# Optimization experiments

Hardware: AMD Instinct MI355X
Metric: run time of the kernel (lower is better)

Reference implementation:

```python
import jax, jax.numpy as jnp
import numpy as np

# dims
B, N = 8, 64            # graphs, nodes per graph (equal-size ragged batch)
IN_DIM, EDGE_DIM = 16, 8
D, H = 128, 4
DH = D // H             # 32
L = 3                   # num_layers
FF = 4 * D              # 512
OUT = 1
SCALE = float(np.sqrt(DH))


def setup_inputs() -> dict:
    key = jax.random.key(0)
    ks = jax.random.split(key, 24)
    w = lambda k, s: jax.random.normal(k, s, jnp.float32) * 0.02
    return {
        'x': jax.random.normal(ks[0], (B, N, IN_DIM), jnp.float32),
        'edge_attr': jax.random.normal(ks[1], (B, N, N, EDGE_DIM), jnp.float32),
        'edge_mask': jax.random.bernoulli(ks[2], 0.2, (B, N, N)),
        # feature encoder (linear node + linear edge encoders, learned no-edge token)
        'node_W': w(ks[3], (IN_DIM, D)), 'node_b': jnp.zeros((D,), jnp.float32),
        'edge_W': w(ks[4], (EDGE_DIM, D)), 'edge_b': jnp.zeros((D,), jnp.float32),
        'no_edge': w(ks[5], (D,)),
        # per-layer edge-transformer params (stacked over L for lax.scan)
        'Wq': w(ks[6], (L, D, D)), 'Wk': w(ks[7], (L, D, D)),
        'Wv1': w(ks[8], (L, D, D)), 'Wv2': w(ks[9], (L, D, D)),
        'Wo': w(ks[10], (L, D, D)), 'bo': jnp.zeros((L, D), jnp.float32),
        'ln1_g': jnp.ones((L, D), jnp.float32), 'ln1_b': jnp.zeros((L, D), jnp.float32),
        'W1': w(ks[11], (L, D, FF)), 'b1': jnp.zeros((L, FF), jnp.float32),
        'W2': w(ks[12], (L, FF, D)), 'b2': jnp.zeros((L, D), jnp.float32),
        'ln2_g': jnp.ones((L, D), jnp.float32), 'ln2_b': jnp.zeros((L, D), jnp.float32),
        'Wout': w(ks[13], (D, OUT)), 'bout': jnp.zeros((OUT,), jnp.float32),
    }


def _ln(t, g, b):
    m = t.mean(-1, keepdims=True)
    v = t.var(-1, keepdims=True)
    return (t - m) * jax.lax.rsqrt(v + 1e-5) * g + b


def _forward(x, edge_attr, edge_mask, node_W, node_b, edge_W, edge_b, no_edge,
             Wq, Wk, Wv1, Wv2, Wo, bo, ln1_g, ln1_b, W1, b1, W2, b2,
             ln2_g, ln2_b, Wout, bout):
    # feature encoding: pair-token grid [B,N,N,D]
    node_emb = x @ node_W + node_b                       # [B,N,D]
    edge_emb = edge_attr @ edge_W + edge_b               # [B,N,N,D]
    tok = jnp.where(edge_mask[..., None], edge_emb, no_edge)
    eye = jnp.eye(N, dtype=bool)
    tok = jnp.where(eye[None, :, :, None], node_emb[:, :, None, :], tok)

    def heads(t, W):
        return (t @ W).reshape(B, N, N, H, DH)

    def layer(tok, p):
        wq, wk, wv1, wv2, wo, bo_, g1, b1_, w1, bf1, w2, bf2, g2, b2_ = p
        q = heads(tok, wq); k = heads(tok, wk)
        v1 = heads(tok, wv1); v2 = heads(tok, wv2)
        # triangular attention: token (i,j) attends over intermediate l
        s = jnp.einsum('bilhd,bljhd->bhilj', q, k) / SCALE   # [B,H,N,N,N]
        a = jax.nn.softmax(s, axis=3)                        # softmax over l
        o = jnp.einsum('bhilj,bilhd,bljhd->bijhd', a, v1, v2).reshape(B, N, N, D)
        tok = _ln(tok + o @ wo + bo_, g1, b1_)
        f = jax.nn.relu(tok @ w1 + bf1) @ w2 + bf2
        tok = _ln(tok + f, g2, b2_)
        return tok, None

    tok, _ = jax.lax.scan(
        layer, tok,
        (Wq, Wk, Wv1, Wv2, Wo, bo, ln1_g, ln1_b, W1, b1, W2, b2, ln2_g, ln2_b))

    diag = tok[:, jnp.arange(N), jnp.arange(N), :]           # node tokens [B,N,D]
    return diag @ Wout + bout                                 # [B,N,OUT]


def reference(x, edge_attr, edge_mask, node_W, node_b, edge_W, edge_b, no_edge,
              Wq, Wk, Wv1, Wv2, Wo, bo, ln1_g, ln1_b, W1, b1, W2, b2,
              ln2_g, ln2_b, Wout, bout):
    return _forward(x, edge_attr, edge_mask, node_W, node_b, edge_W, edge_b,
                    no_edge, Wq, Wk, Wv1, Wv2, Wo, bo, ln1_g, ln1_b,
                    W1, b1, W2, b2, ln2_g, ln2_b, Wout, bout)
```

## Files before the change

kernel.cpp:

```cpp
#include <hip/hip_runtime.h>

typedef unsigned short u16;
typedef __attribute__((ext_vector_type(8))) short bf16x8;
typedef __attribute__((ext_vector_type(4))) float f32x4;

#define INV_SCALE 0.17677669529663687f

static __device__ __forceinline__ float b2f(u16 u) {
    union { unsigned int i; float f; } v; v.i = ((unsigned int)u) << 16; return v.f;
}
static __device__ __forceinline__ u16 f2b(float f) {
    union { float f; unsigned int i; } v; v.f = f;
    unsigned int r = (v.i + 0x7FFFu + ((v.i >> 16) & 1u)) >> 16;
    return (u16)r;
}

#define NSEG 23
__device__ __constant__ int d_seg_off[NSEG + 1] = {
    0, 8192, 270336, 272384, 272512, 273536, 273664, 273792, 322944, 372096,
    421248, 470400, 519552, 519936, 520320, 520704, 717312, 718848, 915456,
    915840, 916224, 916608, 916736, 916744};
static const int h_seg_off[NSEG + 1] = {
    0, 8192, 270336, 272384, 272512, 273536, 273664, 273792, 322944, 372096,
    421248, 470400, 519552, 519936, 520320, 520704, 717312, 718848, 915456,
    915840, 916224, 916608, 916736, 916744};
#define ARENA_TOTAL 916744

struct ParamPtrs { const void* p[NSEG]; };

__global__ __launch_bounds__(256) void convert_params(ParamPtrs pp, u16* __restrict__ arena,
                                                      const void* __restrict__ mask,
                                                      int* __restrict__ mode) {
    if (blockIdx.x == 0) {
        __shared__ int f16, f32s, u8s;
        int tid = threadIdx.x;
        if (tid == 0) { f16 = 0; f32s = 0; u8s = 0; }
        __syncthreads();
        const u16* mu = (const u16*)mask;
        const unsigned int* mw = (const unsigned int*)mask;
        if (mu[2 * tid] == 0x3F80u) atomicOr(&f16, 1);
        if (mw[tid] == 0x3F800000u) atomicOr(&f32s, 1);
        if (mw[tid] > 1u) atomicOr(&u8s, 1);
        __syncthreads();
        if (tid == 0) mode[0] = f16 ? 0 : (f32s ? 3 : (u8s ? 1 : 2));
    }
    const unsigned int probe = ((const unsigned int*)pp.p[13])[0];
    const bool f32 = (probe == 0x3F800000u);
    for (int e = blockIdx.x * 256 + threadIdx.x; e < ARENA_TOTAL; e += gridDim.x * 256) {
        int k = 0;
        #pragma unroll
        for (int s2 = 1; s2 < NSEG; ++s2) if (e >= d_seg_off[s2]) k = s2;
        int local = e - d_seg_off[k];
        u16 v;
        if (k == 22 && local >= 1) v = 0;
        else v = f32 ? f2b(((const float*)pp.p[k])[local]) : ((const u16*)pp.p[k])[local];
        arena[e] = v;
    }
}

__global__ __launch_bounds__(256) void assemble_kernel(
    const u16* __restrict__ x, const u16* __restrict__ ea,
    const void* __restrict__ mask, const int* __restrict__ modeptr,
    const u16* __restrict__ nodeW, const u16* __restrict__ nodeB,
    const u16* __restrict__ edgeW, const u16* __restrict__ edgeB, const u16* __restrict__ noedge,
    float* __restrict__ tokf, u16* __restrict__ tokb)
{
    const int md = modeptr[0];
    int g = blockIdx.x * 256 + threadIdx.x;
    int t = g >> 5, dq = g & 31, d0 = dq * 4;
    int b = t >> 12, i = (t >> 6) & 63, j = t & 63;
    float v[4];
    if (i == j) {
        #pragma unroll
        for (int c = 0; c < 4; c++) v[c] = b2f(nodeB[d0 + c]);
        #pragma unroll
        for (int e = 0; e < 16; e++) {
            float xe = b2f(x[(b * 64 + i) * 16 + e]);
            #pragma unroll
            for (int c = 0; c < 4; c++) v[c] += xe * b2f(nodeW[e * 128 + d0 + c]);
        }
    } else {
        bool edge;
        if (md == 0)      edge = ((const u16*)mask)[t] != 0;
        else if (md == 3) edge = ((const float*)mask)[t] != 0.0f;
        else if (md == 1) edge = ((const unsigned char*)mask)[t] != 0;
        else              edge = ((const unsigned int*)mask)[t] != 0;
        if (edge) {
            #pragma unroll
            for (int c = 0; c < 4; c++) v[c] = b2f(edgeB[d0 + c]);
            #pragma unroll
            for (int e = 0; e < 8; e++) {
                float ae = b2f(ea[t * 8 + e]);
                #pragma unroll
                for (int c = 0; c < 4; c++) v[c] += ae * b2f(edgeW[e * 128 + d0 + c]);
            }
        } else {
            #pragma unroll
            for (int c = 0; c < 4; c++) v[c] = b2f(noedge[d0 + c]);
        }
    }
    *(float4*)(tokf + (size_t)t * 128 + d0) = make_float4(v[0], v[1], v[2], v[3]);
    u16 pk[4];
    #pragma unroll
    for (int c = 0; c < 4; c++) pk[c] = f2b(v[c]);
    *(uint2*)(tokb + (size_t)t * 128 + d0) = *(uint2*)pk;
}

__global__ __launch_bounds__(256) void gemm_kernel(
    const u16* __restrict__ A, int lda,
    const u16* __restrict__ B0, const u16* __restrict__ B1,
    const u16* __restrict__ B2, const u16* __restrict__ B3,
    int ldb, const u16* __restrict__ bias,
    int K, int mode,
    u16* __restrict__ outb, int ldc,
    float* __restrict__ tokf,
    u16* __restrict__ qb, u16* __restrict__ kb, u16* __restrict__ v2b,
    const u16* __restrict__ lng, const u16* __restrict__ lnb, u16* __restrict__ tokbO)
{
    __shared__ __align__(16) u16 smem[2 * 128 * 72];
    u16* As = smem;
    u16* Bs = smem + 128 * 72;
    int tid = threadIdx.x;
    int m0 = blockIdx.x * 128;
    int by = blockIdx.y;
    const u16* Bp; int c0;
    if (mode == 3) { Bp = (by == 0) ? B0 : (by == 1) ? B1 : (by == 2) ? B2 : B3; c0 = 0; }
    else { Bp = B0; c0 = by * 128; }

    int w = tid >> 6, lane = tid & 63;
    int q = lane >> 4, r16 = lane & 15;
    int rw = (w >> 1) * 64, cw = (w & 1) * 64;

    f32x4 acc[4][4];
    #pragma unroll
    for (int mi = 0; mi < 4; mi++)
        #pragma unroll
        for (int ni = 0; ni < 4; ni++) acc[mi][ni] = (f32x4){0.f, 0.f, 0.f, 0.f};

    int nkt = K >> 6;
    for (int kt = 0; kt < nkt; ++kt) {
        int k0 = kt * 64;
        __syncthreads();
        #pragma unroll
        for (int it = 0; it < 4; ++it) {
            int idx = tid + it * 256;
            int row = idx >> 3, ch = idx & 7;
            uint4 d = *(const uint4*)(A + (size_t)(m0 + row) * lda + k0 + ch * 8);
            *(uint4*)&As[row * 72 + ch * 8] = d;
        }
        #pragma unroll
        for (int it = 0; it < 4; ++it) {
            int idx = tid + it * 256;
            int kk = idx >> 4, nc = idx & 15;
            uint4 d = *(const uint4*)(Bp + (size_t)(k0 + kk) * ldb + c0 + nc * 8);
            const u16* ds = (const u16*)&d;
            int chunk = kk >> 3, kin = kk & 7;
            #pragma unroll
            for (int e = 0; e < 8; ++e) {
                int n = nc * 8 + e;
                int ch2 = chunk ^ ((n >> 3) & 7);
                Bs[n * 72 + ch2 * 8 + kin] = ds[e];
            }
        }
        __syncthreads();
        #pragma unroll
        for (int ks = 0; ks < 2; ++ks) {
            bf16x8 fa[4], fb[4];
            #pragma unroll
            for (int mi = 0; mi < 4; mi++)
                fa[mi] = *(const bf16x8*)&As[(rw + mi * 16 + r16) * 72 + ks * 32 + q * 8];
            #pragma unroll
            for (int ni = 0; ni < 4; ni++) {
                int n = cw + ni * 16 + r16;
                int ch2 = (ks * 4 + q) ^ ((n >> 3) & 7);
                fb[ni] = *(const bf16x8*)&Bs[n * 72 + ch2 * 8];
            }
            #pragma unroll
            for (int mi = 0; mi < 4; mi++)
                #pragma unroll
                for (int ni = 0; ni < 4; ni++)
                    acc[mi][ni] = __builtin_amdgcn_mfma_f32_16x16x32_bf16(fa[mi], fb[ni], acc[mi][ni], 0, 0, 0);
        }
    }

    int bl = m0 >> 12, it0 = (m0 >> 6) & 63;
    __syncthreads();
    if (mode == 4) {
        float* cf  = (float*)smem;
        float* rsm = cf + 128 * 64;
        float* rqm = rsm + 256;
        int half = cw >> 6;
        #pragma unroll
        for (int ni = 0; ni < 4; ni++) {
            int col = cw + ni * 16 + r16;
            float bb = b2f(bias[col]);
            #pragma unroll
            for (int mi = 0; mi < 4; mi++)
                #pragma unroll
                for (int rr = 0; rr < 4; rr++) {
                    int r = rw + mi * 16 + q * 4 + rr;
                    acc[mi][ni][rr] += bb + tokf[(size_t)(m0 + r) * 128 + col];
                }
        }
        #pragma unroll
        for (int mi = 0; mi < 4; mi++)
            #pragma unroll
            for (int rr = 0; rr < 4; rr++) {
                float s = 0.f, sq = 0.f;
                #pragma unroll
                for (int ni = 0; ni < 4; ni++) { float t = acc[mi][ni][rr]; s += t; sq += t * t; }
                #pragma unroll
                for (int off = 1; off < 16; off <<= 1) {
                    s  += __shfl_xor(s,  off, 16);
                    sq += __shfl_xor(sq, off, 16);
                }
                if (r16 == 0) {
                    int r = rw + mi * 16 + q * 4 + rr;
                    rsm[half * 128 + r] = s;
                    rqm[half * 128 + r] = sq;
                }
            }
        __syncthreads();
        float gl[4], bv[4];
        #pragma unroll
        for (int ni = 0; ni < 4; ni++) {
            int col = cw + ni * 16 + r16;
            gl[ni] = b2f(lng[col]);
            bv[ni] = b2f(lnb[col]);
        }
        #pragma unroll
        for (int mi = 0; mi < 4; mi++)
            #pragma unroll
            for (int rr = 0; rr < 4; rr++) {
                int r = rw + mi * 16 + q * 4 + rr;
                float tot = rsm[r] + rsm[128 + r];
                float tq  = rqm[r] + rqm[128 + r];
                float mean = tot * 0.0078125f;
                float var  = tq * 0.0078125f - mean * mean;
                float rstd = rsqrtf(var + 1e-5f);
                #pragma unroll
                for (int ni = 0; ni < 4; ni++)
                    acc[mi][ni][rr] = (acc[mi][ni][rr] - mean) * rstd * gl[ni] + bv[ni];
            }
        #pragma unroll
        for (int hp = 0; hp < 2; ++hp) {
            __syncthreads();
            if (half == hp) {
                #pragma unroll
                for (int mi = 0; mi < 4; mi++)
                    #pragma unroll
                    for (int ni = 0; ni < 4; ni++) {
                        int colh = (cw & 63) + ni * 16 + r16;
                        int ch4 = colh >> 2, cl = colh & 3;
                        #pragma unroll
                        for (int rr = 0; rr < 4; rr++) {
                            int r = rw + mi * 16 + q * 4 + rr;
                            cf[r * 64 + (((ch4 ^ (r & 15)) << 2) | cl)] = acc[mi][ni][rr];
                        }
                    }
            }
            __syncthreads();
            #pragma unroll
            for (int it = 0; it < 8; ++it) {
                int idx = tid + it * 256;
                int r = idx >> 4, c4 = idx & 15;
                f32x4 v = *(const f32x4*)&cf[r * 64 + ((c4 ^ (r & 15)) << 2)];
                int col = hp * 64 + c4 * 4;
                *(f32x4*)(tokf + (size_t)(m0 + r) * 128 + col) = v;
                u16 pk[4];
                #pragma unroll
                for (int e = 0; e < 4; e++) pk[e] = f2b(v[e]);
                *(uint2*)(tokbO + (size_t)(m0 + r) * 128 + col) = *(uint2*)pk;
            }
        }
    } else if (mode == 3 && by == 2) {
        float* cf = (float*)smem;
        #pragma unroll
        for (int hp = 0; hp < 2; ++hp) {
            if (hp) __syncthreads();
            if ((cw >> 6) == hp) {
                #pragma unroll
                for (int mi = 0; mi < 4; mi++) {
                    #pragma unroll
                    for (int ni = 0; ni < 4; ni++) {
                        int colh = (cw & 63) + ni * 16 + r16;
                        int ch4 = colh >> 2, cl = colh & 3;
                        #pragma unroll
                        for (int rr = 0; rr < 4; rr++) {
                            int r = rw + mi * 16 + q * 4 + rr;
                            cf[r * 64 + (((ch4 ^ (r & 15)) << 2) | cl)] = acc[mi][ni][rr];
                        }
                    }
                }
            }
            __syncthreads();
            #pragma unroll
            for (int it = 0; it < 8; ++it) {
                int idx = tid + it * 256;
                int hh = idx >> 10, itl = (idx >> 9) & 1, jt = (idx >> 3) & 63, d4 = idx & 7;
                int r = itl * 64 + jt;
                int colh = hh * 32 + d4 * 4;
                f32x4 v = *(const f32x4*)&cf[r * 64 + (((colh >> 2) ^ (r & 15)) << 2)];
                int h = hp * 2 + hh;
                *(f32x4*)&tokf[((((size_t)(bl * 4 + h)) * 64 + it0 + itl) * 64 + jt) * 32 + d4 * 4] = v;
            }
        }
    } else {
        u16* cs = smem;
        #pragma unroll
        for (int mi = 0; mi < 4; mi++) {
            #pragma unroll
            for (int ni = 0; ni < 4; ni++) {
                int col = cw + ni * 16 + r16;
                int ch = col >> 3, cl = col & 7;
                #pragma unroll
                for (int rr = 0; rr < 4; rr++) {
                    int r = rw + mi * 16 + q * 4 + rr;
                    float v = acc[mi][ni][rr];
                    if (mode == 1) { v += b2f(bias[c0 + col]); v = fmaxf(v, 0.f); }
                    cs[r * 128 + (((ch ^ (r & 15)) << 3) | cl)] = f2b(v);
                }
            }
        }
        __syncthreads();
        if (mode == 1) {
            #pragma unroll
            for (int it = 0; it < 8; ++it) {
                int idx = tid + it * 256;
                int r = idx >> 4, c8 = idx & 15;
                uint4 d = *(const uint4*)&cs[r * 128 + ((c8 ^ (r & 15)) << 3)];
                *(uint4*)&outb[(size_t)(m0 + r) * ldc + c0 + c8 * 8] = d;
            }
        } else if (by == 0) {
            #pragma unroll
            for (int it = 0; it < 8; ++it) {
                int idx = tid + it * 256;
                int h = idx >> 9, jt = (idx >> 3) & 63, itl = (idx >> 2) & 1, d8 = idx & 3;
                int r = itl * 64 + jt, c8 = h * 4 + d8;
                uint4 d = *(const uint4*)&cs[r * 128 + ((c8 ^ (r & 15)) << 3)];
                *(uint4*)&qb[((((size_t)(bl * 4 + h)) * 64 + jt) * 64 + it0 + itl) * 32 + d8 * 8] = d;
            }
        } else {
            u16* dp = (by == 1) ? kb : v2b;
            #pragma unroll
            for (int it = 0; it < 8; ++it) {
                int idx = tid + it * 256;
                int h = idx >> 9, itl = (idx >> 8) & 1, jt = (idx >> 2) & 63, d8 = idx & 3;
                int r = itl * 64 + jt, c8 = h * 4 + d8;
                uint4 d = *(const uint4*)&cs[r * 128 + ((c8 ^ (r & 15)) << 3)];
                *(uint4*)&dp[((((size_t)(bl * 4 + h)) * 64 + it0 + itl) * 64 + jt) * 32 + d8 * 8] = d;
            }
        }
    }
}

__global__ __launch_bounds__(64) void attn_s_kernel(
    const u16* __restrict__ qb, const u16* __restrict__ kb, u16* __restrict__ s)
{
    __shared__ __align__(16) u16 qs[64 * 40];
    __shared__ __align__(16) u16 ks_[64 * 40];
    int g = blockIdx.x;
    int l = g & 63, bh = g >> 6;
    const u16* Q = qb + ((size_t)bh * 64 + l) * 2048;
    const u16* Kp = kb + ((size_t)bh * 64 + l) * 2048;
    int lane = threadIdx.x;
    #pragma unroll
    for (int it = 0; it < 4; ++it) {
        int idx = lane + it * 64;
        int row = idx >> 2, c4 = idx & 3;
        *(uint4*)&qs[row * 40 + c4 * 8] = *(const uint4*)(Q + row * 32 + c4 * 8);
        *(uint4*)&ks_[row * 40 + c4 * 8] = *(const uint4*)(Kp + row * 32 + c4 * 8);
    }
    __syncthreads();
    int q = lane >> 4, r16 = lane & 15;
    f32x4 acc[4][4];
    #pragma unroll
    for (int mi = 0; mi < 4; mi++)
        #pragma unroll
        for (int ni = 0; ni < 4; ni++) acc[mi][ni] = (f32x4){0.f, 0.f, 0.f, 0.f};
    bf16x8 fa[4], fb[4];
    #pragma unroll
    for (int mi = 0; mi < 4; mi++) fa[mi] = *(const bf16x8*)&qs[(mi * 16 + r16) * 40 + q * 8];
    #pragma unroll
    for (int ni = 0; ni < 4; ni++) fb[ni] = *(const bf16x8*)&ks_[(ni * 16 + r16) * 40 + q * 8];
    #pragma unroll
    for (int mi = 0; mi < 4; mi++)
        #pragma unroll
        for (int ni = 0; ni < 4; ni++)
            acc[mi][ni] = __builtin_amdgcn_mfma_f32_16x16x32_bf16(fa[mi], fb[ni], acc[mi][ni], 0, 0, 0);
    u16* sb = s + (size_t)bh * 262144 + l * 64;
    #pragma unroll
    for (int mi = 0; mi < 4; mi++)
        #pragma unroll
        for (int ni = 0; ni < 4; ni++)
            #pragma unroll
            for (int rr = 0; rr < 4; rr++) {
                int i = mi * 16 + q * 4 + rr, j = ni * 16 + r16;
                sb[(size_t)i * 4096 + j] = f2b(acc[mi][ni][rr] * INV_SCALE);
            }
}

__global__ __launch_bounds__(512) void attn_o_kernel(
    const u16* __restrict__ a, const float* __restrict__ v1f, const u16* __restrict__ v2b,
    u16* __restrict__ ob)
{
    __shared__ __align__(16) float v2s[4 * 2304];
    __shared__ __align__(16) u16   as_[8 * 4 * 64];
    __shared__ __align__(16) float v1s[8 * 4 * 32];
    int bh = blockIdx.x;
    int i0 = blockIdx.y * 8;
    int bl = bh >> 2, h = bh & 3;
    int tid = threadIdx.x;
    int w = __builtin_amdgcn_readfirstlane(tid >> 6);
    int j = tid & 63;
    int ih = w & 1;
    int dh = (w >> 1) * 8;
    const u16*   v2base = v2b + (size_t)bh * 131072;
    const float* v1base = v1f + (size_t)bh * 131072 + (size_t)i0 * 2048;
    const u16*   abase  = a + (size_t)bh * 262144 + (size_t)i0 * 4096;

    uint4 pv2[2]; unsigned pa[2]; float pv1[2];
    int ia[2], la[2], ja[2], iv[2], lv[2], dv[2], lz[2], jz[2], cz[2];
    #pragma unroll
    for (int it = 0; it < 2; ++it) {
        int idx = tid + it * 512;
        lz[it] = idx >> 8; jz[it] = (idx >> 2) & 63; cz[it] = idx & 3;
        ia[it] = idx >> 7; la[it] = (idx >> 5) & 3; ja[it] = idx & 31;
        iv[it] = idx >> 7; lv[it] = (idx >> 5) & 3; dv[it] = idx & 31;
    }

#define LOAD_CHUNK(l0_)                                                             \
    _Pragma("unroll")                                                               \
    for (int it = 0; it < 2; ++it) {                                                \
        pv2[it] = *(const uint4*)(v2base + ((size_t)((l0_) + lz[it]) * 64 + jz[it]) * 32 + cz[it] * 8); \
        pa[it]  = *(const unsigned*)(abase + (size_t)ia[it] * 4096 + ((l0_) + la[it]) * 64 + ja[it] * 2); \
        pv1[it] = v1base[(size_t)iv[it] * 2048 + ((l0_) + lv[it]) * 32 + dv[it]];   \
    }

#define STORE_CHUNK()                                                               \
    _Pragma("unroll")                                                               \
    for (int it = 0; it < 2; ++it) {                                                \
        const u16* ds = (const u16*)&pv2[it];                                       \
        float* dst = &v2s[lz[it] * 2304 + jz[it] * 36 + cz[it] * 8];                \
        _Pragma("unroll")                                                           \
        for (int e = 0; e < 8; e++) dst[e] = b2f(ds[e]);                            \
        *(unsigned*)&as_[ia[it] * 256 + la[it] * 64 + ja[it] * 2] = pa[it];         \
        v1s[iv[it] * 128 + lv[it] * 32 + dv[it]] = pv1[it];                         \
    }

    float acc[4][8];
    float Z[4];
    #pragma unroll
    for (int i = 0; i < 4; i++) {
        Z[i] = 0.f;
        #pragma unroll
        for (int e = 0; e < 8; e++) acc[i][e] = 0.f;
    }

    LOAD_CHUNK(0);
    for (int ch = 0; ch < 16; ++ch) {
        if (ch) __syncthreads();
        STORE_CHUNK();
        if (ch + 1 < 16) LOAD_CHUNK((ch + 1) * 4);
        __syncthreads();
        #pragma unroll
        for (int lc = 0; lc < 4; ++lc) {
            const float* vp = &v2s[lc * 2304 + j * 36 + dh];
            float v2r[8];
            *(f32x4*)&v2r[0] = *(const f32x4*)vp;
            *(f32x4*)&v2r[4] = *(const f32x4*)(vp + 4);
            #pragma unroll
            for (int ii = 0; ii < 4; ++ii) {
                int iL = ih * 4 + ii;
                float sv = b2f(as_[iL * 256 + lc * 64 + j]);
                float av = __expf(sv);
                Z[ii] += av;
                const float* v1p = &v1s[iL * 128 + lc * 32 + dh];
                #pragma unroll
                for (int e = 0; e < 8; e++)
                    acc[ii][e] += (av * v1p[e]) * v2r[e];
            }
        }
    }
#undef LOAD_CHUNK
#undef STORE_CHUNK

    #pragma unroll
    for (int ii = 0; ii < 4; ++ii) {
        int iL = ih * 4 + ii;
        float sc = 1.0f / Z[ii];
        u16 tmp[8];
        #pragma unroll
        for (int e = 0; e < 8; e++) tmp[e] = f2b(acc[ii][e] * sc);
        *(uint4*)(ob + ((size_t)(bl * 64 + i0 + iL) * 64 + j) * 128 + h * 32 + dh) = *(uint4*)tmp;
    }
}

__global__ __launch_bounds__(256) void out_kernel(
    const float* __restrict__ tokf, const u16* __restrict__ Wout, const u16* __restrict__ bout,
    float* __restrict__ out)
{
    int g = blockIdx.x * 256 + threadIdx.x;
    int b = g >> 6, i = g & 63;
    const float* p = tokf + ((size_t)(b * 64 + i) * 64 + i) * 128;
    float s = b2f(bout[0]);
    #pragma unroll
    for (int d = 0; d < 128; d++) s += p[d] * b2f(Wout[d]);
    out[g] = s;
}

extern "C" void kernel_launch(void* const* d_in, const int* in_sizes, int n_in,
                              void* d_out, int out_size, void* d_ws, size_t ws_size,
                              hipStream_t stream) {
    const void* mask = d_in[2];
    ParamPtrs pp;
    for (int k = 0; k < NSEG; ++k) pp.p[k] = d_in[k < 2 ? k : k + 1];

    char* ws = (char*)d_ws;
    u16* arena = (u16*)ws;
    #define AP(k) ((const u16*)ws + h_seg_off[k])
    int*   mmode = (int*)(ws + 1835008);
    float* tokf  = (float*)(ws + 2097152);
    u16*   tokb  = (u16*)(ws + 18874368);
    const size_t base = 27262976;
    const size_t MB = 1048576ULL;

    int NB = 8;
    while (NB > 1 && base + (size_t)NB * 7 * MB > ws_size) NB >>= 1;
    int F = 1;
    while (F < 8 && base + (size_t)(32768 / F) * 1024ULL > ws_size) F <<= 1;

    u16*   qb  = (u16*)(ws + base);
    u16*   kb  = (u16*)(ws + base + (size_t)NB * MB);
    u16*   v2b = (u16*)(ws + base + (size_t)NB * 2 * MB);
    float* v1f = (float*)(ws + base + (size_t)NB * 3 * MB);
    u16*   sb  = (u16*)(ws + base + (size_t)NB * 5 * MB);
    u16*   ob  = qb;
    u16*   ffb = qb;

    convert_params<<<1024, 256, 0, stream>>>(pp, arena, mask, mmode);
    assemble_kernel<<<4096, 256, 0, stream>>>(AP(0), AP(1), mask, mmode,
                                              AP(2), AP(3), AP(4), AP(5), AP(6), tokf, tokb);

    for (int l = 0; l < 3; ++l) {
        const u16* Wq_l  = AP(7)  + l * 16384;
        const u16* Wk_l  = AP(8)  + l * 16384;
        const u16* Wv1_l = AP(9)  + l * 16384;
        const u16* Wv2_l = AP(10) + l * 16384;
        const u16* Wo_l  = AP(11) + l * 16384;
        const u16* bo_l  = AP(12) + l * 128;
        const u16* g1_l  = AP(13) + l * 128;
        const u16* be1_l = AP(14) + l * 128;
        const u16* W1_l  = AP(15) + l * 65536;
        const u16* b1_l  = AP(16) + l * 512;
        const u16* W2_l  = AP(17) + l * 65536;
        const u16* b2_l  = AP(18) + l * 128;
        const u16* g2_l  = AP(19) + l * 128;
        const u16* be2_l = AP(20) + l * 128;

        for (int r = 0; r < 8 / NB; ++r) {
            size_t rowOff = (size_t)r * NB * 4096;
            gemm_kernel<<<dim3(NB * 32, 4), 256, 0, stream>>>(
                tokb + rowOff * 128, 128, Wq_l, Wk_l, Wv1_l, Wv2_l,
                128, (const u16*)0, 128, 3, (u16*)0, 0, v1f, qb, kb, v2b,
                (const u16*)0, (const u16*)0, (u16*)0);
            attn_s_kernel<<<NB * 256, 64, 0, stream>>>(qb, kb, sb);
            attn_o_kernel<<<dim3(NB * 4, 8), 512, 0, stream>>>(sb, v1f, v2b, ob);
            gemm_kernel<<<dim3(NB * 32, 1), 256, 0, stream>>>(
                ob, 128, Wo_l, (const u16*)0, (const u16*)0, (const u16*)0,
                128, bo_l, 128, 4, (u16*)0, 0, tokf + rowOff * 128,
                (u16*)0, (u16*)0, (u16*)0,
                g1_l, be1_l, tokb + rowOff * 128);
        }
        for (int f = 0; f < F; ++f) {
            size_t r0 = (size_t)f * (32768 / F);
            int RB = (32768 / F) / 128;
            gemm_kernel<<<dim3(RB, 4), 256, 0, stream>>>(
                tokb + r0 * 128, 128, W1_l, (const u16*)0, (const u16*)0, (const u16*)0,
                512, b1_l, 128, 1, ffb, 512, (float*)0, (u16*)0, (u16*)0, (u16*)0,
                (const u16*)0, (const u16*)0, (u16*)0);
            gemm_kernel<<<dim3(RB, 1), 256, 0, stream>>>(
                ffb, 512, W2_l, (const u16*)0, (const u16*)0, (const u16*)0,
                128, b2_l, 512, 4, (u16*)0, 0, tokf + r0 * 128,
                (u16*)0, (u16*)0, (u16*)0,
                g2_l, be2_l, tokb + r0 * 128);
        }
    }
    out_kernel<<<2, 256, 0, stream>>>(tokf, AP(21), AP(22), (float*)d_out);
}
```

Before: 477.6 us.

## Fuse FFN up/down GEMMs with LayerNorm and stage attention scores through LDS

Replaces the two separate FFN GEMM launches with a single ff_kernel. For each 128-row tile it computes the hidden activations in 128-column slices, applies bias and ReLU in shared memory and immediately accumulates the W2 product. Bias, residual and LayerNorm are done in the epilogue, which removes the 32768x512 intermediate buffer's global write and read. Separately, attn_s_kernel now stages the score tile through LDS so it can write coalesced 16-byte rows instead of scattered 2-byte stores. The fused kernel issues only 256 blocks and reloads weights per tile, which may limit occupancy and add redundant weight traffic.

```diff
diff --git a/kernel.cpp b/kernel.cpp
--- a/kernel.cpp
+++ b/kernel.cpp
@@ -316,22 +316,12 @@
                 #pragma unroll
                 for (int rr = 0; rr < 4; rr++) {
                     int r = rw + mi * 16 + q * 4 + rr;
-                    float v = acc[mi][ni][rr];
-                    if (mode == 1) { v += b2f(bias[c0 + col]); v = fmaxf(v, 0.f); }
-                    cs[r * 128 + (((ch ^ (r & 15)) << 3) | cl)] = f2b(v);
-                }
-            }
-        }
-        __syncthreads();
-        if (mode == 1) {
-            #pragma unroll
-            for (int it = 0; it < 8; ++it) {
-                int idx = tid + it * 256;
-                int r = idx >> 4, c8 = idx & 15;
-                uint4 d = *(const uint4*)&cs[r * 128 + ((c8 ^ (r & 15)) << 3)];
-                *(uint4*)&outb[(size_t)(m0 + r) * ldc + c0 + c8 * 8] = d;
-            }
-        } else if (by == 0) {
+                    cs[r * 128 + (((ch ^ (r & 15)) << 3) | cl)] = f2b(acc[mi][ni][rr]);
+                }
+            }
+        }
+        __syncthreads();
+        if (by == 0) {
             #pragma unroll
             for (int it = 0; it < 8; ++it) {
                 int idx = tid + it * 256;
@@ -354,11 +344,228 @@
     }
 }
 
+__global__ __launch_bounds__(256) void ff_kernel(
+    const u16* __restrict__ A,
+    const u16* __restrict__ W1, const u16* __restrict__ b1,
+    const u16* __restrict__ W2, const u16* __restrict__ b2,
+    const u16* __restrict__ lng, const u16* __restrict__ lnb,
+    float* __restrict__ tokf, u16* __restrict__ tokbO)
+{
+    __shared__ __align__(16) u16 smem[2 * 128 * 72];
+    u16* As = smem;
+    u16* Bs = smem + 128 * 72;
+    int tid = threadIdx.x;
+    int m0 = blockIdx.x * 128;
+    int w = tid >> 6, lane = tid & 63;
+    int q = lane >> 4, r16 = lane & 15;
+    int rw = (w >> 1) * 64, cw = (w & 1) * 64;
+
+    f32x4 acc2[4][4];
+    #pragma unroll
+    for (int mi = 0; mi < 4; mi++)
+        #pragma unroll
+        for (int ni = 0; ni < 4; ni++) acc2[mi][ni] = (f32x4){0.f, 0.f, 0.f, 0.f};
+
+    for (int hs = 0; hs < 4; ++hs) {
+        f32x4 acc1[4][4];
+        #pragma unroll
+        for (int mi = 0; mi < 4; mi++)
+            #pragma unroll
+            for (int ni = 0; ni < 4; ni++) acc1[mi][ni] = (f32x4){0.f, 0.f, 0.f, 0.f};
+        #pragma unroll
+        for (int kt = 0; kt < 2; ++kt) {
+            int k0 = kt * 64;
+            __syncthreads();
+            #pragma unroll
+            for (int it = 0; it < 4; ++it) {
+                int idx = tid + it * 256;
+                int row = idx >> 3, ch = idx & 7;
+                uint4 d = *(const uint4*)(A + (size_t)(m0 + row) * 128 + k0 + ch * 8);
+                *(uint4*)&As[row * 72 + ch * 8] = d;
+            }
+            #pragma unroll
+            for (int it = 0; it < 4; ++it) {
+                int idx = tid + it * 256;
+                int kk = idx >> 4, nc = idx & 15;
+                uint4 d = *(const uint4*)(W1 + (size_t)(k0 + kk) * 512 + hs * 128 + nc * 8);
+                const u16* ds = (const u16*)&d;
+                int chunk = kk >> 3, kin = kk & 7;
+                #pragma unroll
+                for (int e = 0; e < 8; ++e) {
+                    int n = nc * 8 + e;
+                    int ch2 = chunk ^ ((n >> 3) & 7);
+                    Bs[n * 72 + ch2 * 8 + kin] = ds[e];
+                }
+            }
+            __syncthreads();
+            #pragma unroll
+            for (int ks = 0; ks < 2; ++ks) {
+                bf16x8 fa[4], fb[4];
+                #pragma unroll
+                for (int mi = 0; mi < 4; mi++)
+                    fa[mi] = *(const bf16x8*)&As[(rw + mi * 16 + r16) * 72 + ks * 32 + q * 8];
+                #pragma unroll
+                for (int ni = 0; ni < 4; ni++) {
+                    int n = cw + ni * 16 + r16;
+                    int ch2 = (ks * 4 + q) ^ ((n >> 3) & 7);
+                    fb[ni] = *(const bf16x8*)&Bs[n * 72 + ch2 * 8];
+                }
+                #pragma unroll
+                for (int mi = 0; mi < 4; mi++)
+                    #pragma unroll
+                    for (int ni = 0; ni < 4; ni++)
+                        acc1[mi][ni] = __builtin_amdgcn_mfma_f32_16x16x32_bf16(fa[mi], fb[ni], acc1[mi][ni], 0, 0, 0);
+            }
+        }
+        #pragma unroll
+        for (int half = 0; half < 2; ++half) {
+            __syncthreads();
+            if ((w & 1) == half) {
+                #pragma unroll
+                for (int mi = 0; mi < 4; mi++)
+                    #pragma unroll
+                    for (int ni = 0; ni < 4; ni++) {
+                        int kl = ni * 16 + r16;
+                        float bb = b2f(b1[hs * 128 + half * 64 + kl]);
+                        #pragma unroll
+                        for (int rr = 0; rr < 4; rr++) {
+                            int row = rw + mi * 16 + q * 4 + rr;
+                            As[row * 72 + kl] = f2b(fmaxf(acc1[mi][ni][rr] + bb, 0.f));
+                        }
+                    }
+            }
+            #pragma unroll
+            for (int it = 0; it < 4; ++it) {
+                int idx = tid + it * 256;
+                int kk = idx >> 4, nc = idx & 15;
+                uint4 d = *(const uint4*)(W2 + (size_t)(hs * 128 + half * 64 + kk) * 128 + nc * 8);
+                const u16* ds = (const u16*)&d;
+                int chunk = kk >> 3, kin = kk & 7;
+                #pragma unroll
+                for (int e = 0; e < 8; ++e) {
+                    int n = nc * 8 + e;
+                    int ch2 = chunk ^ ((n >> 3) & 7);
+                    Bs[n * 72 + ch2 * 8 + kin] = ds[e];
+                }
+            }
+            __syncthreads();
+            #pragma unroll
+            for (int ks = 0; ks < 2; ++ks) {
+                bf16x8 fa[4], fb[4];
+                #pragma unroll
+                for (int mi = 0; mi < 4; mi++)
+                    fa[mi] = *(const bf16x8*)&As[(rw + mi * 16 + r16) * 72 + ks * 32 + q * 8];
+                #pragma unroll
+                for (int ni = 0; ni < 4; ni++) {
+                    int n = cw + ni * 16 + r16;
+                    int ch2 = (ks * 4 + q) ^ ((n >> 3) & 7);
+                    fb[ni] = *(const bf16x8*)&Bs[n * 72 + ch2 * 8];
+                }
+                #pragma unroll
+                for (int mi = 0; mi < 4; mi++)
+                    #pragma unroll
+                    for (int ni = 0; ni < 4; ni++)
+                        acc2[mi][ni] = __builtin_amdgcn_mfma_f32_16x16x32_bf16(fa[mi], fb[ni], acc2[mi][ni], 0, 0, 0);
+            }
+        }
+    }
+
+    __syncthreads();
+    float* cf  = (float*)smem;
+    float* rsm = cf + 128 * 64;
+    float* rqm = rsm + 256;
+    int half = cw >> 6;
+    #pragma unroll
+    for (int ni = 0; ni < 4; ni++) {
+        int col = cw + ni * 16 + r16;
+        float bb = b2f(b2[col]);
+        #pragma unroll
+        for (int mi = 0; mi < 4; mi++)
+            #pragma unroll
+            for (int rr = 0; rr < 4; rr++) {
+                int r = rw + mi * 16 + q * 4 + rr;
+                acc2[mi][ni][rr] += bb + tokf[(size_t)(m0 + r) * 128 + col];
+            }
+    }
+    #pragma unroll
+    for (int mi = 0; mi < 4; mi++)
+        #pragma unroll
+        for (int rr = 0; rr < 4; rr++) {
+            float s = 0.f, sq = 0.f;
+            #pragma unroll
+            for (int ni = 0; ni < 4; ni++) { float t = acc2[mi][ni][rr]; s += t; sq += t * t; }
+            #pragma unroll
+            for (int off = 1; off < 16; off <<= 1) {
+                s  += __shfl_xor(s,  off, 16);
+                sq += __shfl_xor(sq, off, 16);
+            }
+            if (r16 == 0) {
+                int r = rw + mi * 16 + q * 4 + rr;
+                rsm[half * 128 + r] = s;
+                rqm[half * 128 + r] = sq;
+            }
+        }
+    __syncthreads();
+    float gl[4], bv[4];
+    #pragma unroll
+    for (int ni = 0; ni < 4; ni++) {
+        int col = cw + ni * 16 + r16;
+        gl[ni] = b2f(lng[col]);
+        bv[ni] = b2f(lnb[col]);
+    }
+    #pragma unroll
+    for (int mi = 0; mi < 4; mi++)
+        #pragma unroll
+        for (int rr = 0; rr < 4; rr++) {
+            int r = rw + mi * 16 + q * 4 + rr;
+            float tot = rsm[r] + rsm[128 + r];
+            float tq  = rqm[r] + rqm[128 + r];
+            float mean = tot * 0.0078125f;
+            float var  = tq * 0.0078125f - mean * mean;
+            float rstd = rsqrtf(var + 1e-5f);
+            #pragma unroll
+            for (int ni = 0; ni < 4; ni++)
+                acc2[mi][ni][rr] = (acc2[mi][ni][rr] - mean) * rstd * gl[ni] + bv[ni];
+        }
+    #pragma unroll
+    for (int hp = 0; hp < 2; ++hp) {
+        __syncthreads();
+        if (half == hp) {
+            #pragma unroll
+            for (int mi = 0; mi < 4; mi++)
+                #pragma unroll
+                for (int ni = 0; ni < 4; ni++) {
+                    int colh = (cw & 63) + ni * 16 + r16;
+                    int ch4 = colh >> 2, cl = colh & 3;
+                    #pragma unroll
+                    for (int rr = 0; rr < 4; rr++) {
+                        int r = rw + mi * 16 + q * 4 + rr;
+                        cf[r * 64 + (((ch4 ^ (r & 15)) << 2) | cl)] = acc2[mi][ni][rr];
+                    }
+                }
+        }
+        __syncthreads();
+        #pragma unroll
+        for (int it = 0; it < 8; ++it) {
+            int idx = tid + it * 256;
+            int r = idx >> 4, c4 = idx & 15;
+            f32x4 v = *(const f32x4*)&cf[r * 64 + ((c4 ^ (r & 15)) << 2)];
+            int col = hp * 64 + c4 * 4;
+            *(f32x4*)(tokf + (size_t)(m0 + r) * 128 + col) = v;
+            u16 pk[4];
+            #pragma unroll
+            for (int e = 0; e < 4; e++) pk[e] = f2b(v[e]);
+            *(uint2*)(tokbO + (size_t)(m0 + r) * 128 + col) = *(uint2*)pk;
+        }
+    }
+}
+
 __global__ __launch_bounds__(64) void attn_s_kernel(
     const u16* __restrict__ qb, const u16* __restrict__ kb, u16* __restrict__ s)
 {
-    __shared__ __align__(16) u16 qs[64 * 40];
-    __shared__ __align__(16) u16 ks_[64 * 40];
+    __shared__ __align__(16) u16 sm[64 * 80];
+    u16* qs  = sm;
+    u16* ks_ = sm + 64 * 40;
     int g = blockIdx.x;
     int l = g & 63, bh = g >> 6;
     const u16* Q = qb + ((size_t)bh * 64 + l) * 2048;
@@ -388,16 +595,23 @@
         #pragma unroll
         for (int ni = 0; ni < 4; ni++)
             acc[mi][ni] = __builtin_amdgcn_mfma_f32_16x16x32_bf16(fa[mi], fb[ni], acc[mi][ni], 0, 0, 0);
+    __syncthreads();
+    u16* cs = sm;
+    #pragma unroll
+    for (int mi = 0; mi < 4; mi++)
+        #pragma unroll
+        for (int ni = 0; ni < 4; ni++)
+            #pragma unroll
+            for (int rr = 0; rr < 4; rr++)
+                cs[(mi * 16 + q * 4 + rr) * 72 + ni * 16 + r16] = f2b(acc[mi][ni][rr] * INV_SCALE);
+    __syncthreads();
     u16* sb = s + (size_t)bh * 262144 + l * 64;
     #pragma unroll
-    for (int mi = 0; mi < 4; mi++)
-        #pragma unroll
-        for (int ni = 0; ni < 4; ni++)
-            #pragma unroll
-            for (int rr = 0; rr < 4; rr++) {
-                int i = mi * 16 + q * 4 + rr, j = ni * 16 + r16;
-                sb[(size_t)i * 4096 + j] = f2b(acc[mi][ni][rr] * INV_SCALE);
-            }
+    for (int it = 0; it < 8; ++it) {
+        int row = it * 8 + (lane >> 3);
+        uint4 d = *(const uint4*)&cs[row * 72 + (lane & 7) * 8];
+        *(uint4*)&sb[(size_t)row * 4096 + (lane & 7) * 8] = d;
+    }
 }
 
 __global__ __launch_bounds__(512) void attn_o_kernel(
@@ -527,8 +741,6 @@
 
     int NB = 8;
     while (NB > 1 && base + (size_t)NB * 7 * MB > ws_size) NB >>= 1;
-    int F = 1;
-    while (F < 8 && base + (size_t)(32768 / F) * 1024ULL > ws_size) F <<= 1;
 
     u16*   qb  = (u16*)(ws + base);
     u16*   kb  = (u16*)(ws + base + (size_t)NB * MB);
@@ -536,7 +748,6 @@
     float* v1f = (float*)(ws + base + (size_t)NB * 3 * MB);
     u16*   sb  = (u16*)(ws + base + (size_t)NB * 5 * MB);
     u16*   ob  = qb;
-    u16*   ffb = qb;
 
     convert_params<<<1024, 256, 0, stream>>>(pp, arena, mask, mmode);
     assemble_kernel<<<4096, 256, 0, stream>>>(AP(0), AP(1), mask, mmode,
@@ -572,19 +783,8 @@
                 (u16*)0, (u16*)0, (u16*)0,
                 g1_l, be1_l, tokb + rowOff * 128);
         }
-        for (int f = 0; f < F; ++f) {
-            size_t r0 = (size_t)f * (32768 / F);
-            int RB = (32768 / F) / 128;
-            gemm_kernel<<<dim3(RB, 4), 256, 0, stream>>>(
-                tokb + r0 * 128, 128, W1_l, (const u16*)0, (const u16*)0, (const u16*)0,
-                512, b1_l, 128, 1, ffb, 512, (float*)0, (u16*)0, (u16*)0, (u16*)0,
-                (const u16*)0, (const u16*)0, (u16*)0);
-            gemm_kernel<<<dim3(RB, 1), 256, 0, stream>>>(
-                ffb, 512, W2_l, (const u16*)0, (const u16*)0, (const u16*)0,
-                128, b2_l, 512, 4, (u16*)0, 0, tokf + r0 * 128,
-                (u16*)0, (u16*)0, (u16*)0,
-                g2_l, be2_l, tokb + r0 * 128);
-        }
+        ff_kernel<<<256, 256, 0, stream>>>(tokb, W1_l, b1_l, W2_l, b2_l,
+                                           g2_l, be2_l, tokf, tokb);
     }
     out_kernel<<<2, 256, 0, stream>>>(tokf, AP(21), AP(22), (float*)d_out);
 }
```

New measurement: 438.1 us. -8.3%, faster.
